# Optimization experiments

Measured on AMD Instinct MI355X. Metric: run time of the kernel, lower is better.

## Reference

```python
import jax, jax.numpy as jnp
import numpy as np


def setup_inputs() -> dict:
    key = jax.random.key(0)
    k1, k2, k3 = jax.random.split(key, 3)
    B, S, D, H = 16, 4096, 512, 512
    inp = jax.random.normal(k1, (B, S, D), dtype=jnp.float32)
    # torch nn.Linear(D, 3*H): weight (3H, D), bias (3H,)
    W = jax.random.normal(k2, (3 * H, D), dtype=jnp.float32) * (1.0 / np.sqrt(D))
    b = jax.random.normal(k3, (3 * H,), dtype=jnp.float32) * 0.01
    return {"inp": inp, "W": W, "b": b}


def _forget_mult(z, f):
    # z, f: (B, S, H). h_t = f_t*z_t + (1-f_t)*h_{t-1}, h_{-1}=0 (hid=None)
    zt = jnp.swapaxes(z, 0, 1)  # (S, B, H)
    ft = jnp.swapaxes(f, 0, 1)
    h0 = jnp.zeros(z.shape[0:1] + z.shape[2:3], dtype=z.dtype)  # (B, H)

    def step(h, zf):
        zi, fi = zf
        h = fi * zi + (1.0 - fi) * h
        return h, h

    _, hs = jax.lax.scan(step, h0, (zt, ft))
    return jnp.swapaxes(hs, 0, 1)  # (B, S, H)


def reference(inp, W, b):
    # QRNNLayer forward: window=1, output_gate=True, batch_first=True,
    # backward=False, zoneout=0, hid=None.
    y = jnp.einsum('bsd,hd->bsh', inp, W) + b  # (B, S, 3H)
    z_gate, f_gate, o_gate = jnp.split(y, 3, axis=2)
    z_gate = jnp.tanh(z_gate)
    f_gate = jax.nn.sigmoid(f_gate)
    c_gate = _forget_mult(z_gate, f_gate)
    output = jax.nn.sigmoid(o_gate) * c_gate
    return output, c_gate[:, -1]
```

## Files before the change

### kernel.cpp

```cpp
#include <hip/hip_runtime.h>
#include <stdint.h>

#define Bdim 16
#define Sdim 4096
#define Hdim 512
#define Mdim (Bdim*Sdim)
#define N3   (3*Hdim)
#define Kdim 512
#define NCHUNK 64
#define CLEN  (Sdim/NCHUNK)

typedef __bf16 bf16;
typedef __bf16 bf16x4 __attribute__((ext_vector_type(4)));
typedef __bf16 bf16x8 __attribute__((ext_vector_type(8)));
typedef float  f32x4  __attribute__((ext_vector_type(4)));
typedef _Float16 f16;
typedef _Float16 f16x4 __attribute__((ext_vector_type(4)));
typedef _Float16 f16x8 __attribute__((ext_vector_type(8)));

__device__ __forceinline__ void gload_lds16(const void* g, void* l) {
  __builtin_amdgcn_global_load_lds(
      (const __attribute__((address_space(1))) uint32_t*)g,
      (__attribute__((address_space(3))) uint32_t*)l, 16, 0, 0);
}

__global__ void __launch_bounds__(256) cvt_kernel(const float4* __restrict__ in,
                                                  bf16x4* __restrict__ out, int n4) {
  int i = blockIdx.x * blockDim.x + threadIdx.x;
  if (i >= n4) return;
  float4 v = in[i];
  bf16x4 o;
  o.x = (bf16)v.x; o.y = (bf16)v.y; o.z = (bf16)v.z; o.w = (bf16)v.w;
  out[i] = o;
}

#define BM 256
#define BN 256
#define BK2 32
#define NT (Kdim/BK2)

__global__ void __launch_bounds__(512, 2) gemm_act_kernel(
    const bf16* __restrict__ A, const bf16* __restrict__ Wb,
    const float* __restrict__ bias,
    f16* __restrict__ zbuf, f16* __restrict__ fbuf, f16* __restrict__ ogbuf) {
  __shared__ char lds[131072];
  const int tid  = threadIdx.x;
  const int wid  = tid >> 6;
  const int lane = tid & 63;
  const int wr = wid >> 2, wc = wid & 3;
  const int bid = blockIdx.x;
  const int wg  = (bid & 7) * 192 + (bid >> 3);
  const int mt = wg / (N3 / BN);
  const int nt = wg % (N3 / BN);
  const int row0 = mt * BM;

  const bf16* Ag = A  + (size_t)row0 * Kdim;
  const bf16* Bg = Wb + (size_t)(nt * BN) * Kdim;

  uint32_t srcO[2];
  {
    int rlo = tid >> 2, spos = tid & 3;
    #pragma unroll
    for (int i = 0; i < 2; ++i) {
      int row = i * 128 + rlo;
      srcO[i] = (uint32_t)(row * Kdim + ((spos ^ ((row >> 1) & 3)) << 3));
    }
  }
  const uint32_t dstBase = (uint32_t)(wid * 1024);

  uint32_t byteA[8], byteB[4];
  {
    int kslot = lane >> 4;
    #pragma unroll
    for (int m = 0; m < 8; ++m) {
      int row = wr * 128 + m * 16 + (lane & 15);
      byteA[m] = (uint32_t)(row * 64 + ((kslot ^ ((row >> 1) & 3)) << 4));
    }
    #pragma unroll
    for (int n = 0; n < 4; ++n) {
      int row = wc * 64 + n * 16 + (lane & 15);
      byteB[n] = (uint32_t)(16384 + row * 64 + ((kslot ^ ((row >> 1) & 3)) << 4));
    }
  }

  f32x4 acc[8][4];
  #pragma unroll
  for (int m = 0; m < 8; ++m)
    #pragma unroll
    for (int n = 0; n < 4; ++n)
      acc[m][n] = (f32x4){0.f, 0.f, 0.f, 0.f};

  #pragma unroll
  for (int kt = 0; kt < 3; ++kt) {
    char* ring = lds + kt * 32768;
    #pragma unroll
    for (int i = 0; i < 2; ++i)
      gload_lds16(Ag + srcO[i] + kt * BK2, ring + i * 8192 + dstBase);
    #pragma unroll
    for (int i = 0; i < 2; ++i)
      gload_lds16(Bg + srcO[i] + kt * BK2, ring + 16384 + i * 8192 + dstBase);
  }
  asm volatile("s_waitcnt vmcnt(8)" ::: "memory");
  __builtin_amdgcn_s_barrier();
  __builtin_amdgcn_sched_barrier(0);

  #pragma unroll
  for (int t = 0; t < NT; ++t) {
    if (t + 3 < NT) {
      char* ring = lds + ((t + 3) & 3) * 32768;
      #pragma unroll
      for (int i = 0; i < 2; ++i)
        gload_lds16(Ag + srcO[i] + (t + 3) * BK2, ring + i * 8192 + dstBase);
      #pragma unroll
      for (int i = 0; i < 2; ++i)
        gload_lds16(Bg + srcO[i] + (t + 3) * BK2, ring + 16384 + i * 8192 + dstBase);
    }
    const char* Ab = lds + (t & 3) * 32768;
    bf16x8 af[8], bfrag[4];
    #pragma unroll
    for (int m = 0; m < 8; ++m) af[m] = *(const bf16x8*)(Ab + byteA[m]);
    #pragma unroll
    for (int n = 0; n < 4; ++n) bfrag[n] = *(const bf16x8*)(Ab + byteB[n]);
    __builtin_amdgcn_s_setprio(1);
    #pragma unroll
    for (int m = 0; m < 8; ++m)
      #pragma unroll
      for (int n = 0; n < 4; ++n)
        acc[m][n] = __builtin_amdgcn_mfma_f32_16x16x32_bf16(af[m], bfrag[n], acc[m][n], 0, 0, 0);
    __builtin_amdgcn_s_setprio(0);
    if (t <= NT - 4) {
      asm volatile("s_waitcnt vmcnt(8)" ::: "memory");
    } else if (t == NT - 3) {
      asm volatile("s_waitcnt vmcnt(4)" ::: "memory");
    } else if (t == NT - 2) {
      asm volatile("s_waitcnt vmcnt(0)" ::: "memory");
    }
    if (t < NT - 1) {
      __builtin_amdgcn_s_barrier();
      __builtin_amdgcn_sched_barrier(0);
    }
  }

  __syncthreads();

  const int gate = nt >> 1;
  const int cb   = (nt & 1) * 256;
  f16* dst = (gate == 0) ? zbuf : ((gate == 1) ? fbuf : ogbuf);
  float bv[4];
  #pragma unroll
  for (int n = 0; n < 4; ++n)
    bv[n] = bias[gate * Hdim + cb + wc * 64 + n * 16 + (lane & 15)];

  #pragma unroll
  for (int m = 0; m < 8; ++m) {
    #pragma unroll
    for (int n = 0; n < 4; ++n) {
      int col = wc * 64 + n * 16 + (lane & 15);
      #pragma unroll
      for (int r = 0; r < 4; ++r) {
        int row = wr * 128 + m * 16 + (lane >> 4) * 4 + r;
        float y = acc[m][n][r] + bv[n];
        float v;
        if (gate == 0) {
          float e = __expf(2.f * y);
          v = 1.f - 2.f / (e + 1.f);
        } else {
          v = 1.f / (1.f + __expf(-y));
        }
        uint32_t byte = (uint32_t)(row * 512 + col * 2) ^ ((uint32_t)(row & 7) << 4);
        *(f16*)(lds + byte) = (f16)v;
      }
    }
  }
  __syncthreads();
  #pragma unroll
  for (int j = 0; j < 16; ++j) {
    int c = j * 512 + tid;
    int row = c >> 5, col8 = c & 31;
    uint32_t byte = (uint32_t)(row * 512 + col8 * 16) ^ ((uint32_t)(row & 7) << 4);
    f16x8 v = *(const f16x8*)(lds + byte);
    *(f16x8*)&dst[(size_t)(row0 + row) * Hdim + cb + col8 * 8] = v;
  }
}

__global__ void __launch_bounds__(256) scanA_kernel(const f16x4* __restrict__ z4,
                                                    const f16x4* __restrict__ f4,
                                                    float* __restrict__ Pb,
                                                    float* __restrict__ Qb) {
  int u  = blockIdx.x * blockDim.x + threadIdx.x;
  int hq = u & 127;
  int bc = u >> 7;
  int b  = bc & (Bdim - 1);
  int c  = bc >> 4;
  size_t base = ((size_t)(b * Sdim + c * CLEN)) * 128 + hq;
  float P[4] = {1.f, 1.f, 1.f, 1.f}, Q[4] = {0.f, 0.f, 0.f, 0.f};
  #pragma unroll 4
  for (int s = 0; s < CLEN; ++s) {
    f16x4 fv = f4[base], zv = z4[base];
    #pragma unroll
    for (int j = 0; j < 4; ++j) {
      float f = (float)fv[j];
      Q[j] += f * ((float)zv[j] - Q[j]);
      P[j] *= (1.f - f);
    }
    base += 128;
  }
  int outi = ((c * Bdim + b) << 9) + hq * 4;
  *(float4*)&Pb[outi] = make_float4(P[0], P[1], P[2], P[3]);
  *(float4*)&Qb[outi] = make_float4(Q[0], Q[1], Q[2], Q[3]);
}

__global__ void __launch_bounds__(256) scanB_kernel(const float* __restrict__ Pb,
                                                    const float* __restrict__ Qb,
                                                    float* __restrict__ hin,
                                                    float* __restrict__ c_last) {
  int t = blockIdx.x * blockDim.x + threadIdx.x;
  int h = t & (Hdim - 1), b = t >> 9;
  float hs = 0.f;
  #pragma unroll 8
  for (int c = 0; c < NCHUNK; ++c) {
    hin[c * (Bdim * Hdim) + t] = hs;
    int u = ((c * Bdim + b) << 9) + h;
    hs = Pb[u] * hs + Qb[u];
  }
  c_last[t] = hs;
}

__global__ void __launch_bounds__(256) scanC_kernel(const f16x4* __restrict__ z4,
                                                    const f16x4* __restrict__ f4,
                                                    const f16x4* __restrict__ og4,
                                                    const float* __restrict__ hin,
                                                    float4* __restrict__ out4) {
  int u  = blockIdx.x * blockDim.x + threadIdx.x;
  int hq = u & 127;
  int bc = u >> 7;
  int b  = bc & (Bdim - 1);
  int c  = bc >> 4;
  float4 hv = *(const float4*)&hin[c * (Bdim * Hdim) + b * Hdim + hq * 4];
  float h[4] = {hv.x, hv.y, hv.z, hv.w};
  size_t base = ((size_t)(b * Sdim + c * CLEN)) * 128 + hq;
  #pragma unroll 4
  for (int s = 0; s < CLEN; ++s) {
    f16x4 fv = f4[base], zv = z4[base], ov = og4[base];
    float4 o;
    #pragma unroll
    for (int j = 0; j < 4; ++j) {
      h[j] += (float)fv[j] * ((float)zv[j] - h[j]);
    }
    o.x = (float)ov[0] * h[0]; o.y = (float)ov[1] * h[1];
    o.z = (float)ov[2] * h[2]; o.w = (float)ov[3] * h[3];
    out4[base] = o;
    base += 128;
  }
}

extern "C" void kernel_launch(void* const* d_in, const int* in_sizes, int n_in,
                              void* d_out, int out_size, void* d_ws, size_t ws_size,
                              hipStream_t stream) {
  const float* inp  = (const float*)d_in[0];
  const float* W    = (const float*)d_in[1];
  const float* bias = (const float*)d_in[2];
  float* out = (float*)d_out;

  char* ws = (char*)d_ws;
  bf16* Abf = (bf16*)(ws);
  bf16* Wbf = (bf16*)(ws + 67108864);
  f16*  zh  = (f16*) (ws + 68681728);
  f16*  fh  = (f16*) (ws + 135790592);
  f16*  ogh = (f16*) (ws + 202899456);
  float* Pb = (float*)(ws + 270008320);
  float* Qb = (float*)(ws + 272105472);
  float* hin= (float*)(ws + 274202624);

  {
    int n4 = (Mdim * Kdim) / 4;
    cvt_kernel<<<n4 / 256, 256, 0, stream>>>((const float4*)inp, (bf16x4*)Abf, n4);
  }
  {
    int n4 = (N3 * Kdim) / 4;
    cvt_kernel<<<n4 / 256, 256, 0, stream>>>((const float4*)W, (bf16x4*)Wbf, n4);
  }
  gemm_act_kernel<<<(Mdim / BM) * (N3 / BN), 512, 0, stream>>>(Abf, Wbf, bias,
                                                               zh, fh, ogh);
  scanA_kernel<<<(NCHUNK * Bdim * 128) / 256, 256, 0, stream>>>(
      (const f16x4*)zh, (const f16x4*)fh, Pb, Qb);
  scanB_kernel<<<(Bdim * Hdim) / 256, 256, 0, stream>>>(Pb, Qb, hin,
                                                        out + (size_t)Mdim * Hdim);
  scanC_kernel<<<(NCHUNK * Bdim * 128) / 256, 256, 0, stream>>>(
      (const f16x4*)zh, (const f16x4*)fh, (const f16x4*)ogh, hin, (float4*)out);
}
```

Before: 312.7 us.

## Shrink GEMM LDS to 64KB with double buffering and two-pass epilogue

Replaces the 4-stage, 128KB LDS prefetch ring in the GEMM with a 2-stage, 64KB double buffer that uses a full __syncthreads each iteration. The activation epilogue is split into two half-tile passes so the fp16 staging fits in the smaller LDS. The likely aim is to free LDS so more workgroups fit per CU (launch bounds ask for 2). In exchange, prefetch depth drops from three tiles to one and every K step now waits on a full barrier, so global-load latency is less hidden.

```diff
diff --git a/kernel.cpp b/kernel.cpp
--- a/kernel.cpp
+++ b/kernel.cpp
@@ -43,7 +43,7 @@
     const bf16* __restrict__ A, const bf16* __restrict__ Wb,
     const float* __restrict__ bias,
     f16* __restrict__ zbuf, f16* __restrict__ fbuf, f16* __restrict__ ogbuf) {
-  __shared__ char lds[131072];
+  __shared__ char lds[65536];
   const int tid  = threadIdx.x;
   const int wid  = tid >> 6;
   const int lane = tid & 63;
@@ -59,11 +59,11 @@
 
   uint32_t srcO[2];
   {
-    int rlo = tid >> 2, spos = tid & 3;
+    int r_ = tid >> 2, slot = tid & 3;
     #pragma unroll
     for (int i = 0; i < 2; ++i) {
-      int row = i * 128 + rlo;
-      srcO[i] = (uint32_t)(row * Kdim + ((spos ^ ((row >> 1) & 3)) << 3));
+      int row = i * 128 + r_;
+      srcO[i] = (uint32_t)(row * Kdim + ((slot ^ ((row >> 1) & 3)) << 3));
     }
   }
   const uint32_t dstBase = (uint32_t)(wid * 1024);
@@ -90,32 +90,26 @@
     for (int n = 0; n < 4; ++n)
       acc[m][n] = (f32x4){0.f, 0.f, 0.f, 0.f};
 
-  #pragma unroll
-  for (int kt = 0; kt < 3; ++kt) {
-    char* ring = lds + kt * 32768;
-    #pragma unroll
-    for (int i = 0; i < 2; ++i)
-      gload_lds16(Ag + srcO[i] + kt * BK2, ring + i * 8192 + dstBase);
-    #pragma unroll
-    for (int i = 0; i < 2; ++i)
-      gload_lds16(Bg + srcO[i] + kt * BK2, ring + 16384 + i * 8192 + dstBase);
-  }
-  asm volatile("s_waitcnt vmcnt(8)" ::: "memory");
-  __builtin_amdgcn_s_barrier();
-  __builtin_amdgcn_sched_barrier(0);
-
-  #pragma unroll
+  {
+    char* Ad = lds; char* Bd = lds + 16384;
+    #pragma unroll
+    for (int i = 0; i < 2; ++i) gload_lds16(Ag + srcO[i], Ad + i * 8192 + dstBase);
+    #pragma unroll
+    for (int i = 0; i < 2; ++i) gload_lds16(Bg + srcO[i], Bd + i * 8192 + dstBase);
+  }
+  __syncthreads();
+
   for (int t = 0; t < NT; ++t) {
-    if (t + 3 < NT) {
-      char* ring = lds + ((t + 3) & 3) * 32768;
+    if (t + 1 < NT) {
+      char* Ad = lds + ((t + 1) & 1) * 32768; char* Bd = Ad + 16384;
       #pragma unroll
       for (int i = 0; i < 2; ++i)
-        gload_lds16(Ag + srcO[i] + (t + 3) * BK2, ring + i * 8192 + dstBase);
+        gload_lds16(Ag + srcO[i] + (t + 1) * BK2, Ad + i * 8192 + dstBase);
       #pragma unroll
       for (int i = 0; i < 2; ++i)
-        gload_lds16(Bg + srcO[i] + (t + 3) * BK2, ring + 16384 + i * 8192 + dstBase);
-    }
-    const char* Ab = lds + (t & 3) * 32768;
+        gload_lds16(Bg + srcO[i] + (t + 1) * BK2, Bd + i * 8192 + dstBase);
+    }
+    const char* Ab = lds + (t & 1) * 32768;
     bf16x8 af[8], bfrag[4];
     #pragma unroll
     for (int m = 0; m < 8; ++m) af[m] = *(const bf16x8*)(Ab + byteA[m]);
@@ -128,58 +122,52 @@
       for (int n = 0; n < 4; ++n)
         acc[m][n] = __builtin_amdgcn_mfma_f32_16x16x32_bf16(af[m], bfrag[n], acc[m][n], 0, 0, 0);
     __builtin_amdgcn_s_setprio(0);
-    if (t <= NT - 4) {
-      asm volatile("s_waitcnt vmcnt(8)" ::: "memory");
-    } else if (t == NT - 3) {
-      asm volatile("s_waitcnt vmcnt(4)" ::: "memory");
-    } else if (t == NT - 2) {
-      asm volatile("s_waitcnt vmcnt(0)" ::: "memory");
-    }
-    if (t < NT - 1) {
-      __builtin_amdgcn_s_barrier();
-      __builtin_amdgcn_sched_barrier(0);
-    }
-  }
-
-  __syncthreads();
+    __syncthreads();
+  }
 
   const int gate = nt >> 1;
-  const int cb   = (nt & 1) * 256;
+  const int cbn  = (nt & 1) * 256;
   f16* dst = (gate == 0) ? zbuf : ((gate == 1) ? fbuf : ogbuf);
   float bv[4];
   #pragma unroll
   for (int n = 0; n < 4; ++n)
-    bv[n] = bias[gate * Hdim + cb + wc * 64 + n * 16 + (lane & 15)];
+    bv[n] = bias[gate * Hdim + cbn + wc * 64 + n * 16 + (lane & 15)];
 
   #pragma unroll
-  for (int m = 0; m < 8; ++m) {
-    #pragma unroll
-    for (int n = 0; n < 4; ++n) {
-      int col = wc * 64 + n * 16 + (lane & 15);
-      #pragma unroll
-      for (int r = 0; r < 4; ++r) {
-        int row = wr * 128 + m * 16 + (lane >> 4) * 4 + r;
-        float y = acc[m][n][r] + bv[n];
-        float v;
-        if (gate == 0) {
-          float e = __expf(2.f * y);
-          v = 1.f - 2.f / (e + 1.f);
-        } else {
-          v = 1.f / (1.f + __expf(-y));
+  for (int R = 0; R < 2; ++R) {
+    #pragma unroll
+    for (int m4 = 0; m4 < 4; ++m4) {
+      const int m = R * 4 + m4;
+      #pragma unroll
+      for (int n = 0; n < 4; ++n) {
+        int col = wc * 64 + n * 16 + (lane & 15);
+        #pragma unroll
+        for (int r = 0; r < 4; ++r) {
+          int Lrow = wr * 64 + m4 * 16 + (lane >> 4) * 4 + r;
+          float y = acc[m][n][r] + bv[n];
+          float v;
+          if (gate == 0) {
+            float e = __expf(2.f * y);
+            v = 1.f - 2.f / (e + 1.f);
+          } else {
+            v = 1.f / (1.f + __expf(-y));
+          }
+          uint32_t byte = (uint32_t)(Lrow * 512 + col * 2) ^ ((uint32_t)(Lrow & 7) << 4);
+          *(f16*)(lds + byte) = (f16)v;
         }
-        uint32_t byte = (uint32_t)(row * 512 + col * 2) ^ ((uint32_t)(row & 7) << 4);
-        *(f16*)(lds + byte) = (f16)v;
       }
     }
-  }
-  __syncthreads();
-  #pragma unroll
-  for (int j = 0; j < 16; ++j) {
-    int c = j * 512 + tid;
-    int row = c >> 5, col8 = c & 31;
-    uint32_t byte = (uint32_t)(row * 512 + col8 * 16) ^ ((uint32_t)(row & 7) << 4);
-    f16x8 v = *(const f16x8*)(lds + byte);
-    *(f16x8*)&dst[(size_t)(row0 + row) * Hdim + cb + col8 * 8] = v;
+    __syncthreads();
+    #pragma unroll
+    for (int j = 0; j < 8; ++j) {
+      int c = j * 512 + tid;
+      int Lrow = c >> 5, col8 = c & 31;
+      uint32_t byte = (uint32_t)(Lrow * 512 + col8 * 16) ^ ((uint32_t)(Lrow & 7) << 4);
+      f16x8 v = *(const f16x8*)(lds + byte);
+      int G = (Lrow >> 6) * 128 + R * 64 + (Lrow & 63);
+      *(f16x8*)&dst[(size_t)(row0 + G) * Hdim + cbn + col8 * 8] = v;
+    }
+    __syncthreads();
   }
 }
 
```

Result: no change. 313.9 us (+0.4%).
